# Optimization experiments

Measured on AMD Instinct MI355X. Metric: run time of the kernel, lower is better.

## Reference

```python
import jax, jax.numpy as jnp
import numpy as np

N = 50000       # nodes
E = 800000      # edges (avg degree 16)
IN = 256        # input features
HEADS = 4
D = 32          # per-head dim (hidden_channels/heads = 128/4)
HID = HEADS * D # 128
OUT = 64        # out_channels, last layer has 1 head
SLOPE = 0.2     # DGL GATConv LeakyReLU negative slope


def setup_inputs() -> dict:
    key = jax.random.key(0)
    ks = jax.random.split(key, 11)
    s = 0.05
    return {
        "x": jax.random.normal(ks[0], (N, IN), jnp.float32),
        "W1": jax.random.normal(ks[1], (IN, HID), jnp.float32) * s,
        "al1": jax.random.normal(ks[2], (HEADS, D), jnp.float32) * s,
        "ar1": jax.random.normal(ks[3], (HEADS, D), jnp.float32) * s,
        "b1": jnp.zeros((HID,), jnp.float32),
        "W2": jax.random.normal(ks[4], (HID, OUT), jnp.float32) * s,
        "al2": jax.random.normal(ks[5], (1, OUT), jnp.float32) * s,
        "ar2": jax.random.normal(ks[6], (1, OUT), jnp.float32) * s,
        "b2": jnp.zeros((OUT,), jnp.float32),
        "src": jax.random.randint(ks[7], (E,), 0, N),
        "dst": jax.random.randint(ks[8], (E,), 0, N),
    }


def gat_conv(h, W, al, ar, b, src, dst, heads, d):
    # h: [N, F_in]; projects, computes edge attention, edge-softmax over dst,
    # scatter-reduce aggregation. Matches dglnn.GATConv (bias, no residual).
    feat = (h @ W).reshape(-1, heads, d)              # [N, H, D]
    el = jnp.einsum('nhd,hd->nh', feat, al)           # [N, H]
    er = jnp.einsum('nhd,hd->nh', feat, ar)           # [N, H]
    e = jax.nn.leaky_relu(el[src] + er[dst], SLOPE)   # [E, H] edge scores
    # edge softmax over incoming edges of each dst node
    m = jax.ops.segment_max(e, dst, num_segments=N)   # [N, H]
    ee = jnp.exp(e - m[dst])                          # [E, H]
    z = jax.ops.segment_sum(ee, dst, num_segments=N)  # [N, H]
    a = ee / z[dst]                                   # [E, H]
    msg = feat[src] * a[:, :, None]                   # [E, H, D] gather + weight
    out = jax.ops.segment_sum(msg, dst, num_segments=N)  # [N, H, D]
    return out + b.reshape(heads, d)


def reference(x, W1, al1, ar1, b1, W2, al2, ar2, b2, src, dst):
    h = gat_conv(x, W1, al1, ar1, b1, src, dst, HEADS, D)   # [N, 4, 32]
    h = jax.nn.relu(h).reshape(N, HID)                      # activation; dropout=identity (eval)
    h = gat_conv(h, W2, al2, ar2, b2, src, dst, 1, OUT)     # [N, 1, 64]
    return h.reshape(N, OUT)
```

## Files before the change

kernel.cpp:

```cpp
#include <hip/hip_runtime.h>
#include <math.h>

#define NN   50000
#define EE   800000
#define INF_ 256
#define HID  128
#define OUTF 64
#define DCAP 96
#define SLOPE 0.2f
#define G1B  782
#define NB   391
#define NCH  196
#define CHCAP 6144

typedef __attribute__((ext_vector_type(8))) short short8v;
typedef __attribute__((ext_vector_type(4))) float f32x4;

__device__ __forceinline__ float lrelu(float x) { return x > 0.f ? x : SLOPE * x; }
__device__ __forceinline__ float4 lrelu4(float4 v) {
  v.x = lrelu(v.x); v.y = lrelu(v.y); v.z = lrelu(v.z); v.w = lrelu(v.w); return v;
}
__device__ __forceinline__ unsigned short f2bf(float x) {
  unsigned int u = __float_as_uint(x);
  unsigned int r = (u + 0x7FFFu + ((u >> 16) & 1u)) >> 16;
  return (unsigned short)r;
}

__global__ __launch_bounds__(256) void convW_k(const float* __restrict__ W1,
                                               const float* __restrict__ W2,
                                               unsigned short* __restrict__ W1T,
                                               unsigned short* __restrict__ W2T,
                                               int* __restrict__ cursor) {
  int t = threadIdx.x;
  if (blockIdx.x == 160) {
    if (t < NCH) cursor[t] = t * CHCAP;
    return;
  }
  int id = blockIdx.x * 256 + t;
  if (id < 32768) {
    int k = id >> 7, c = id & 127;
    W1T[c * 256 + k] = f2bf(W1[k * 128 + c]);
  } else {
    int i2 = id - 32768;
    if (i2 < 8192) {
      int k = i2 >> 6, c = i2 & 63;
      W2T[c * 128 + k] = f2bf(W2[i2]);
    }
  }
}

__global__ __launch_bounds__(256) void scat2_k(const int* __restrict__ src,
                                               const int* __restrict__ dst,
                                               int* __restrict__ cursor,
                                               int* __restrict__ packed) {
  __shared__ int h[NCH];
  __shared__ int cur[NCH];
  int t = threadIdx.x, b = blockIdx.x;
  if (t < NCH) h[t] = 0;
  __syncthreads();
  const int4* d4p = (const int4*)dst;
  const int4* s4p = (const int4*)src;
  int4 d4[2], s4[2];
  bool val[2];
#pragma unroll
  for (int it = 0; it < 2; ++it) {
    int qi = b * 512 + it * 256 + t;
    val[it] = qi < EE / 4;
    if (val[it]) {
      d4[it] = d4p[qi];
      s4[it] = s4p[qi];
      atomicAdd(&h[d4[it].x >> 8], 1);
      atomicAdd(&h[d4[it].y >> 8], 1);
      atomicAdd(&h[d4[it].z >> 8], 1);
      atomicAdd(&h[d4[it].w >> 8], 1);
    }
  }
  __syncthreads();
  if (t < NCH) {
    int c = h[t];
    cur[t] = (c > 0) ? atomicAdd(&cursor[t], c) : 0;
  }
  __syncthreads();
#pragma unroll
  for (int it = 0; it < 2; ++it) {
    if (val[it]) {
      int p, c, lim;
      c = d4[it].x >> 8; lim = (c + 1) * CHCAP;
      p = atomicAdd(&cur[c], 1); if (p < lim) packed[p] = (s4[it].x << 8) | (d4[it].x & 255);
      c = d4[it].y >> 8; lim = (c + 1) * CHCAP;
      p = atomicAdd(&cur[c], 1); if (p < lim) packed[p] = (s4[it].y << 8) | (d4[it].y & 255);
      c = d4[it].z >> 8; lim = (c + 1) * CHCAP;
      p = atomicAdd(&cur[c], 1); if (p < lim) packed[p] = (s4[it].z << 8) | (d4[it].z & 255);
      c = d4[it].w >> 8; lim = (c + 1) * CHCAP;
      p = atomicAdd(&cur[c], 1); if (p < lim) packed[p] = (s4[it].w << 8) | (d4[it].w & 255);
    }
  }
}

__global__ __launch_bounds__(256) void csort_k(const int* __restrict__ packed,
                                               const int* __restrict__ cursor,
                                               int* __restrict__ adj,
                                               int* __restrict__ rowptr,
                                               int* __restrict__ cnt) {
  __shared__ int pk[CHCAP];
  __shared__ int h[256], sc[256], cur[256];
  int t = threadIdx.x, b = blockIdx.x;
  int base = b * CHCAP;
  int len = cursor[b] - base; if (len > CHCAP) len = CHCAP;
  h[t] = 0;
  __syncthreads();
  for (int i = t; i < len; i += 256) {
    int v = packed[base + i];
    pk[i] = v;
    atomicAdd(&h[v & 255], 1);
  }
  __syncthreads();
  int v0 = h[t];
  sc[t] = v0;
  __syncthreads();
  for (int off = 1; off < 256; off <<= 1) {
    int add = (t >= off) ? sc[t - off] : 0;
    __syncthreads();
    sc[t] += add;
    __syncthreads();
  }
  int excl = sc[t] - v0;
  int node = b * 256 + t;
  if (node < NN) { cnt[node] = v0; rowptr[node] = base + excl; }
  cur[t] = excl;
  __syncthreads();
  for (int i = t; i < len; i += 256) {
    int v = pk[i];
    int p = atomicAdd(&cur[v & 255], 1);
    adj[base + p] = v & 0xFFFFFF00;
  }
}

__global__ __launch_bounds__(256) void g1s_k(const float* __restrict__ x,
                                             const unsigned short* __restrict__ W1T,
                                             unsigned short* __restrict__ featb,
                                             const float* __restrict__ al,
                                             const float* __restrict__ ar,
                                             float* __restrict__ el,
                                             float* __restrict__ er) {
  __shared__ unsigned short As[64 * 128];
  __shared__ unsigned short Bs[128 * 128];
  int t = threadIdx.x;
  int lane = t & 63, wid = t >> 6;
  int n0 = blockIdx.x * 64;
  int wr = (wid >> 1) * 32;
  int wc = (wid & 1) * 64;

  f32x4 acc[2][4];
#pragma unroll
  for (int m = 0; m < 2; ++m)
#pragma unroll
    for (int n = 0; n < 4; ++n) acc[m][n] = (f32x4){0.f, 0.f, 0.f, 0.f};

  for (int pass = 0; pass < 2; ++pass) {
    int k0 = pass * 128;
#pragma unroll
    for (int it = 0; it < 8; ++it) {
      int f = it * 256 + t;
      int row = f >> 5;
      int c4  = f & 31;
      int grow = n0 + row;
      float4 v = make_float4(0.f, 0.f, 0.f, 0.f);
      if (grow < NN) v = *(const float4*)&x[grow * INF_ + k0 + c4 * 4];
      ushort4 b4;
      b4.x = f2bf(v.x); b4.y = f2bf(v.y); b4.z = f2bf(v.z); b4.w = f2bf(v.w);
      int byte = row * 256 + c4 * 8;
      byte ^= (row & 15) << 4;
      *(ushort4*)((char*)As + byte) = b4;
    }
#pragma unroll
    for (int it = 0; it < 8; ++it) {
      int f = it * 256 + t;
      int c  = f >> 4;
      int k8 = f & 15;
      uint4 v = *(const uint4*)&W1T[c * 256 + k0 + k8 * 8];
      int byte = c * 256 + k8 * 16;
      byte ^= (c & 15) << 4;
      *(uint4*)((char*)Bs + byte) = v;
    }
    __syncthreads();
#pragma unroll
    for (int ks = 0; ks < 4; ++ks) {
      int kb = ks * 64 + (lane >> 4) * 16;
      short8v a[2], b[4];
#pragma unroll
      for (int m = 0; m < 2; ++m) {
        int row = wr + m * 16 + (lane & 15);
        int byte = (row * 256 + kb) ^ ((row & 15) << 4);
        a[m] = *(const short8v*)((const char*)As + byte);
      }
#pragma unroll
      for (int n = 0; n < 4; ++n) {
        int c = wc + n * 16 + (lane & 15);
        int byte = (c * 256 + kb) ^ ((c & 15) << 4);
        b[n] = *(const short8v*)((const char*)Bs + byte);
      }
#pragma unroll
      for (int m = 0; m < 2; ++m)
#pragma unroll
        for (int n = 0; n < 4; ++n)
          acc[m][n] = __builtin_amdgcn_mfma_f32_16x16x32_bf16(a[m], b[n], acc[m][n], 0, 0, 0);
    }
    __syncthreads();
  }
#pragma unroll
  for (int m = 0; m < 2; ++m) {
    int rbase = wr + m * 16 + (lane >> 4) * 4;
#pragma unroll
    for (int r = 0; r < 4; ++r)
#pragma unroll
      for (int n = 0; n < 4; ++n)
        As[(rbase + r) * 128 + wc + n * 16 + (lane & 15)] = f2bf(acc[m][n][r]);
  }
  __syncthreads();
#pragma unroll
  for (int it = 0; it < 4; ++it) {
    int id = it * 256 + t;
    int row = id >> 4, c8 = id & 15;
    int grow = n0 + row;
    if (grow < NN)
      *(uint4*)&featb[grow * HID + c8 * 8] = *(const uint4*)&As[row * 128 + c8 * 8];
  }
  {
    int row = t >> 2, h = t & 3;
    int grow = n0 + row;
    float pe = 0.f, pr = 0.f;
#pragma unroll
    for (int d = 0; d < 16; ++d) {
      unsigned int u = *(const unsigned int*)&As[row * 128 + h * 32 + d * 2];
      float f0 = __uint_as_float(u << 16);
      float f1 = __uint_as_float(u & 0xFFFF0000u);
      float2 a2 = *(const float2*)&al[h * 32 + d * 2];
      float2 r2 = *(const float2*)&ar[h * 32 + d * 2];
      pe += f0 * a2.x + f1 * a2.y;
      pr += f0 * r2.x + f1 * r2.y;
    }
    if (grow < NN) { el[grow * 4 + h] = pe; er[grow * 4 + h] = pr; }
  }
}

__global__ __launch_bounds__(256) void agg1_k(const unsigned short* __restrict__ featb,
                                              const float* __restrict__ el1,
                                              const float* __restrict__ er1,
                                              const float* __restrict__ b1,
                                              const int* __restrict__ cnt,
                                              const int* __restrict__ rowptr,
                                              const int* __restrict__ adj,
                                              unsigned short* __restrict__ houtb) {
  __shared__ float ee[4][DCAP * 4];
  int wid = threadIdx.x >> 6, lane = threadIdx.x & 63;
  int n = blockIdx.x * 4 + wid;
  int deg = cnt[n]; if (deg > DCAP) deg = DCAP;
  const int* bk = adj + rowptr[n];
  float4 er = *(const float4*)(er1 + n * 4);
  int hl = lane >> 4;
  int m64 = deg < 64 ? deg : 64;
  int myoff = (lane < m64) ? bk[lane] : -1;
  const char* fb = (const char*)featb;
  int lb = lane * 4;

  float4 e4my = make_float4(0.f, 0.f, 0.f, 0.f);
  if (myoff >= 0 && deg <= 64)
    e4my = *(const float4*)((const char*)el1 + (myoff >> 4));
  unsigned int upre[16];
#pragma unroll
  for (int k = 0; k < 16; ++k) {
    int o = __shfl(myoff, k);
    upre[k] = *(const unsigned int*)(fb + ((k < m64) ? o : 0) + lb);
  }
  __builtin_amdgcn_sched_barrier(0);

  if (deg <= 64) {
    float4 ex = make_float4(0.f, 0.f, 0.f, 0.f);
    if (myoff >= 0) {
      float4 sc = lrelu4(make_float4(e4my.x + er.x, e4my.y + er.y,
                                     e4my.z + er.z, e4my.w + er.w));
      ex = make_float4(__expf(sc.x), __expf(sc.y), __expf(sc.z), __expf(sc.w));
    }
    float4 zs = ex;
#pragma unroll
    for (int off = 1; off < 64; off <<= 1) {
      zs.x += __shfl_xor(zs.x, off); zs.y += __shfl_xor(zs.y, off);
      zs.z += __shfl_xor(zs.z, off); zs.w += __shfl_xor(zs.w, off);
    }
    if (myoff >= 0) {
      float4 w = make_float4(ex.x / zs.x, ex.y / zs.y, ex.z / zs.z, ex.w / zs.w);
      *(float4*)&ee[wid][lane * 4] = w;
    }
  } else {
    float4 mx = make_float4(-INFINITY, -INFINITY, -INFINITY, -INFINITY);
    for (int j = lane; j < deg; j += 64) {
      int o = bk[j];
      float4 e4 = *(const float4*)((const char*)el1 + (o >> 4));
      float4 sc = lrelu4(make_float4(e4.x + er.x, e4.y + er.y, e4.z + er.z, e4.w + er.w));
      mx.x = fmaxf(mx.x, sc.x); mx.y = fmaxf(mx.y, sc.y);
      mx.z = fmaxf(mx.z, sc.z); mx.w = fmaxf(mx.w, sc.w);
    }
#pragma unroll
    for (int off = 1; off < 64; off <<= 1) {
      mx.x = fmaxf(mx.x, __shfl_xor(mx.x, off));
      mx.y = fmaxf(mx.y, __shfl_xor(mx.y, off));
      mx.z = fmaxf(mx.z, __shfl_xor(mx.z, off));
      mx.w = fmaxf(mx.w, __shfl_xor(mx.w, off));
    }
    float4 zs = make_float4(0.f, 0.f, 0.f, 0.f);
    for (int j = lane; j < deg; j += 64) {
      int o = bk[j];
      float4 e4 = *(const float4*)((const char*)el1 + (o >> 4));
      float4 sc = lrelu4(make_float4(e4.x + er.x, e4.y + er.y, e4.z + er.z, e4.w + er.w));
      float4 ex = make_float4(__expf(sc.x - mx.x), __expf(sc.y - mx.y),
                              __expf(sc.z - mx.z), __expf(sc.w - mx.w));
      *(float4*)&ee[wid][j * 4] = ex;
      zs.x += ex.x; zs.y += ex.y; zs.z += ex.z; zs.w += ex.w;
    }
#pragma unroll
    for (int off = 1; off < 64; off <<= 1) {
      zs.x += __shfl_xor(zs.x, off); zs.y += __shfl_xor(zs.y, off);
      zs.z += __shfl_xor(zs.z, off); zs.w += __shfl_xor(zs.w, off);
    }
    float4 iz = make_float4(1.f / zs.x, 1.f / zs.y, 1.f / zs.z, 1.f / zs.w);
    for (int j = lane; j < deg; j += 64) {
      float4 t = *(const float4*)&ee[wid][j * 4];
      t.x *= iz.x; t.y *= iz.y; t.z *= iz.z; t.w *= iz.w;
      *(float4*)&ee[wid][j * 4] = t;
    }
  }

  float acc0 = 0.f, acc1 = 0.f;
#pragma unroll
  for (int k = 0; k < 16; ++k) {
    float w = (k < m64) ? ee[wid][k * 4 + hl] : 0.f;
    acc0 += __uint_as_float(upre[k] << 16) * w;
    acc1 += __uint_as_float(upre[k] & 0xFFFF0000u) * w;
  }
  int j = 16;
  for (; j + 16 <= m64; j += 16) {
    unsigned int u[16];
#pragma unroll
    for (int q = 0; q < 16; ++q) {
      int o = __shfl(myoff, j + q);
      u[q] = *(const unsigned int*)(fb + o + lb);
    }
#pragma unroll
    for (int q = 0; q < 16; ++q) {
      float w = ee[wid][(j + q) * 4 + hl];
      acc0 += __uint_as_float(u[q] << 16) * w;
      acc1 += __uint_as_float(u[q] & 0xFFFF0000u) * w;
    }
  }
  for (; j + 4 <= m64; j += 4) {
    unsigned int u[4];
#pragma unroll
    for (int q = 0; q < 4; ++q) {
      int o = __shfl(myoff, j + q);
      u[q] = *(const unsigned int*)(fb + o + lb);
    }
#pragma unroll
    for (int q = 0; q < 4; ++q) {
      float w = ee[wid][(j + q) * 4 + hl];
      acc0 += __uint_as_float(u[q] << 16) * w;
      acc1 += __uint_as_float(u[q] & 0xFFFF0000u) * w;
    }
  }
  for (; j < m64; ++j) {
    int o = __shfl(myoff, j);
    unsigned int u = *(const unsigned int*)(fb + o + lb);
    float w = ee[wid][j * 4 + hl];
    acc0 += __uint_as_float(u << 16) * w; acc1 += __uint_as_float(u & 0xFFFF0000u) * w;
  }
  for (; j < deg; ++j) {
    int o = bk[j];
    unsigned int u = *(const unsigned int*)(fb + o + lb);
    float w = ee[wid][j * 4 + hl];
    acc0 += __uint_as_float(u << 16) * w; acc1 += __uint_as_float(u & 0xFFFF0000u) * w;
  }
  float2 bb = *(const float2*)&b1[lane * 2];
  float o0 = fmaxf(acc0 + bb.x, 0.f);
  float o1 = fmaxf(acc1 + bb.y, 0.f);
  unsigned int p = (unsigned int)f2bf(o0) | ((unsigned int)f2bf(o1) << 16);
  *(unsigned int*)&houtb[n * HID + lane * 2] = p;
}

__global__ __launch_bounds__(256) void gemm2s_mfma(const unsigned short* __restrict__ hb,
                                                   const unsigned short* __restrict__ W2T,
                                                   unsigned short* __restrict__ f2b,
                                                   const float* __restrict__ al2,
                                                   const float* __restrict__ ar2,
                                                   float* __restrict__ el2,
                                                   float* __restrict__ er2) {
  __shared__ char smem[32768];
  __shared__ float pel[64][4], per_[64][4];
  unsigned short* As = (unsigned short*)smem;
  unsigned short* Bs = (unsigned short*)(smem + 16384);
  int t = threadIdx.x, lane = t & 63, wid = t >> 6;
  int n0 = blockIdx.x * 64;
  f32x4 acc[4];
#pragma unroll
  for (int n = 0; n < 4; ++n) acc[n] = (f32x4){0.f, 0.f, 0.f, 0.f};

#pragma unroll
  for (int it = 0; it < 4; ++it) {
    int id = it * 256 + t;
    int row = id >> 4, c8 = id & 15;
    int grow = n0 + row;
    uint4 v = make_uint4(0, 0, 0, 0);
    if (grow < NN) v = *(const uint4*)&hb[grow * HID + c8 * 8];
    int byte = row * 256 + c8 * 16;
    byte ^= (row & 15) << 4;
    *(uint4*)((char*)As + byte) = v;
  }
#pragma unroll
  for (int it = 0; it < 4; ++it) {
    int id = it * 256 + t;
    int row = id >> 4, c8 = id & 15;
    uint4 v = *(const uint4*)&W2T[row * 128 + c8 * 8];
    int byte = row * 256 + c8 * 16;
    byte ^= (row & 15) << 4;
    *(uint4*)((char*)Bs + byte) = v;
  }
  __syncthreads();
  int wr = wid * 16;
#pragma unroll
  for (int ks = 0; ks < 4; ++ks) {
    int kb = ks * 64 + (lane >> 4) * 16;
    int arow = wr + (lane & 15);
    int abyte = (arow * 256 + kb) ^ ((arow & 15) << 4);
    short8v a = *(const short8v*)((const char*)As + abyte);
#pragma unroll
    for (int n = 0; n < 4; ++n) {
      int c = n * 16 + (lane & 15);
      int bbyte = (c * 256 + kb) ^ ((c & 15) << 4);
      short8v b = *(const short8v*)((const char*)Bs + bbyte);
      acc[n] = __builtin_amdgcn_mfma_f32_16x16x32_bf16(a, b, acc[n], 0, 0, 0);
    }
  }
  __syncthreads();
  float* stg = (float*)smem;
  unsigned short* sB = (unsigned short*)(smem + 16640);
  int rloc = wr + (lane >> 4) * 4;
#pragma unroll
  for (int r = 0; r < 4; ++r) {
#pragma unroll
    for (int n = 0; n < 4; ++n) {
      int col = n * 16 + (lane & 15);
      float v = acc[n][r];
      stg[(rloc + r) * 65 + col] = v;
      sB[(rloc + r) * 64 + col] = f2bf(v);
    }
  }
  __syncthreads();
#pragma unroll
  for (int it = 0; it < 2; ++it) {
    int id = it * 256 + t;
    int row = id >> 3, c8 = id & 7;
    int grow = n0 + row;
    if (grow < NN)
      *(uint4*)&f2b[grow * OUTF + c8 * 8] = *(const uint4*)&sB[row * 64 + c8 * 8];
  }
  {
    int row = t >> 2, seg = t & 3;
    float pe = 0.f, pr = 0.f;
#pragma unroll
    for (int d = 0; d < 16; ++d) {
      int c = seg * 16 + d;
      float f = stg[row * 65 + c];
      pe += f * al2[c];
      pr += f * ar2[c];
    }
    pel[row][seg] = pe; per_[row][seg] = pr;
  }
  __syncthreads();
  if (t < 64) {
    int grow = n0 + t;
    if (grow < NN) {
      el2[grow] = pel[t][0] + pel[t][1] + pel[t][2] + pel[t][3];
      er2[grow] = per_[t][0] + per_[t][1] + per_[t][2] + per_[t][3];
    }
  }
}

__global__ __launch_bounds__(256) void agg2_k(const unsigned short* __restrict__ f2b,
                                              const float* __restrict__ el2,
                                              const float* __restrict__ er2,
                                              const float* __restrict__ b2,
                                              const int* __restrict__ cnt,
                                              const int* __restrict__ rowptr,
                                              const int* __restrict__ adj,
                                              float* __restrict__ out) {
  __shared__ float ee[4][DCAP];
  int wid = threadIdx.x >> 6, lane = threadIdx.x & 63;
  int n = blockIdx.x * 4 + wid;
  int deg = cnt[n]; if (deg > DCAP) deg = DCAP;
  const int* bk = adj + rowptr[n];
  float er = er2[n];
  int m64 = deg < 64 ? deg : 64;
  int myoff = (lane < m64) ? bk[lane] : -1;
  int half = lane >> 5, c2 = (lane & 31) * 2;
  const char* fb = (const char*)f2b;

  float elmy = 0.f;
  if (myoff >= 0 && deg <= 64)
    elmy = *(const float*)((const char*)el2 + (myoff >> 6));
  unsigned int upre[8];
#pragma unroll
  for (int s = 0; s < 8; ++s) {
    int je = s * 2 + half;
    int o = __shfl(myoff, je);
    upre[s] = *(const unsigned int*)(fb + ((je < m64) ? (o >> 1) : 0) + c2 * 2);
  }
  __builtin_amdgcn_sched_barrier(0);

  if (deg <= 64) {
    float ex = (myoff >= 0) ? __expf(lrelu(elmy + er)) : 0.f;
    float zs = ex;
#pragma unroll
    for (int off = 1; off < 64; off <<= 1) zs += __shfl_xor(zs, off);
    if (myoff >= 0) ee[wid][lane] = ex / zs;
  } else {
    float mx = -INFINITY;
    for (int j = lane; j < deg; j += 64) {
      int o = bk[j];
      mx = fmaxf(mx, lrelu(*(const float*)((const char*)el2 + (o >> 6)) + er));
    }
#pragma unroll
    for (int off = 1; off < 64; off <<= 1) mx = fmaxf(mx, __shfl_xor(mx, off));
    float zs = 0.f;
    for (int j = lane; j < deg; j += 64) {
      int o = bk[j];
      float ex = __expf(lrelu(*(const float*)((const char*)el2 + (o >> 6)) + er) - mx);
      ee[wid][j] = ex;
      zs += ex;
    }
#pragma unroll
    for (int off = 1; off < 64; off <<= 1) zs += __shfl_xor(zs, off);
    float iz = 1.f / zs;
    for (int j = lane; j < deg; j += 64) ee[wid][j] *= iz;
  }

  float acc0 = 0.f, acc1 = 0.f;
#pragma unroll
  for (int s = 0; s < 8; ++s) {
    int je = s * 2 + half;
    float w = (je < m64) ? ee[wid][je] : 0.f;
    acc0 += __uint_as_float(upre[s] << 16) * w;
    acc1 += __uint_as_float(upre[s] & 0xFFFF0000u) * w;
  }
  int j = 16;
  for (; j + 16 <= deg; j += 16) {
    unsigned int u[8]; float w[8];
#pragma unroll
    for (int q = 0; q < 8; ++q) {
      int je = j + q * 2 + half;
      int os = __shfl(myoff, je < 64 ? je : 63);
      int o = (je < 64) ? os : bk[je];
      u[q] = *(const unsigned int*)(fb + (o >> 1) + c2 * 2);
      w[q] = ee[wid][je];
    }
#pragma unroll
    for (int q = 0; q < 8; ++q) {
      acc0 += __uint_as_float(u[q] << 16) * w[q];
      acc1 += __uint_as_float(u[q] & 0xFFFF0000u) * w[q];
    }
  }
  for (; j < deg; j += 2) {
    int je = j + half;
    int os = __shfl(myoff, (je < 64) ? je : 63);
    float w = 0.f; unsigned int u = 0;
    if (je < deg) {
      int o = (je < 64) ? os : bk[je];
      u = *(const unsigned int*)(fb + (o >> 1) + c2 * 2);
      w = ee[wid][je];
    }
    acc0 += __uint_as_float(u << 16) * w;
    acc1 += __uint_as_float(u & 0xFFFF0000u) * w;
  }
  acc0 += __shfl_xor(acc0, 32);
  acc1 += __shfl_xor(acc1, 32);
  if (lane < 32) {
    float2 bb = *(const float2*)&b2[c2];
    *(float2*)&out[n * OUTF + c2] = make_float2(acc0 + bb.x, acc1 + bb.y);
  }
}

extern "C" void kernel_launch(void* const* d_in, const int* in_sizes, int n_in,
                              void* d_out, int out_size, void* d_ws, size_t ws_size,
                              hipStream_t stream) {
  const float* x   = (const float*)d_in[0];
  const float* W1  = (const float*)d_in[1];
  const float* al1 = (const float*)d_in[2];
  const float* ar1 = (const float*)d_in[3];
  const float* b1  = (const float*)d_in[4];
  const float* W2  = (const float*)d_in[5];
  const float* al2 = (const float*)d_in[6];
  const float* ar2 = (const float*)d_in[7];
  const float* b2  = (const float*)d_in[8];
  const int*   src = (const int*)d_in[9];
  const int*   dst = (const int*)d_in[10];
  float* out = (float*)d_out;

  char* base = (char*)d_ws;
  unsigned short* feat1b = (unsigned short*)base;
  unsigned short* f2b    = (unsigned short*)base;
  int*            packed = (int*)base;
  unsigned short* hb     = (unsigned short*)(base + 12800000);
  float* el1 = (float*)(base + 25600000);
  float* er1 = el1 + NN * 4;
  float* el2 = er1 + NN * 4;
  float* er2 = el2 + NN;
  int* cnt    = (int*)(er2 + NN);
  int* rowptr = cnt + NN;
  int* adj    = rowptr + NN;
  int* cursor = adj + NCH * CHCAP;
  unsigned short* W1T = (unsigned short*)(cursor + NCH);
  unsigned short* W2T = W1T + 256 * 128;

  convW_k <<<161, 256, 0, stream>>>(W1, W2, W1T, W2T, cursor);
  scat2_k <<<NB, 256, 0, stream>>>(src, dst, cursor, packed);
  csort_k <<<NCH, 256, 0, stream>>>(packed, cursor, adj, rowptr, cnt);
  g1s_k   <<<G1B, 256, 0, stream>>>(x, W1T, feat1b, al1, ar1, el1, er1);
  agg1_k  <<<NN / 4, 256, 0, stream>>>(feat1b, el1, er1, b1, cnt, rowptr, adj, hb);
  gemm2s_mfma<<<G1B, 256, 0, stream>>>(hb, W2T, f2b, al2, ar2, el2, er2);
  agg2_k  <<<NN / 4, 256, 0, stream>>>(f2b, el2, er2, b2, cnt, rowptr, adj, out);
}
```

Baseline: 125.9 us.

## Merge graph-prep and GEMM kernels to cut launches and overlap independent work

Fuses the weight conversion into the edge-scatter kernel and the per-chunk counting sort into the first-layer GEMM kernel, selecting the role by block index. The cursor initialization moves to a memset, with cursors now relative to each chunk base. The packed buffer gets its own workspace region instead of aliasing feat1b, because the sort and the GEMM now run concurrently. This removes two launches and lets independent blocks overlap. The cost is one shared 48KB smem allocation per block, which may reduce occupancy for the sort blocks.

```diff
diff --git a/kernel.cpp b/kernel.cpp
--- a/kernel.cpp
+++ b/kernel.cpp
@@ -26,36 +26,32 @@
   return (unsigned short)r;
 }
 
-__global__ __launch_bounds__(256) void convW_k(const float* __restrict__ W1,
-                                               const float* __restrict__ W2,
-                                               unsigned short* __restrict__ W1T,
-                                               unsigned short* __restrict__ W2T,
-                                               int* __restrict__ cursor) {
+__global__ __launch_bounds__(256) void prep_k(const int* __restrict__ src,
+                                              const int* __restrict__ dst,
+                                              int* __restrict__ cursor,
+                                              int* __restrict__ packed,
+                                              const float* __restrict__ W1,
+                                              const float* __restrict__ W2,
+                                              unsigned short* __restrict__ W1T,
+                                              unsigned short* __restrict__ W2T) {
   int t = threadIdx.x;
-  if (blockIdx.x == 160) {
-    if (t < NCH) cursor[t] = t * CHCAP;
+  if (blockIdx.x >= NB) {
+    int id = (blockIdx.x - NB) * 256 + t;
+    if (id < 32768) {
+      int k = id >> 7, c = id & 127;
+      W1T[c * 256 + k] = f2bf(W1[k * 128 + c]);
+    } else {
+      int i2 = id - 32768;
+      if (i2 < 8192) {
+        int k = i2 >> 6, c = i2 & 63;
+        W2T[c * 128 + k] = f2bf(W2[i2]);
+      }
+    }
     return;
   }
-  int id = blockIdx.x * 256 + t;
-  if (id < 32768) {
-    int k = id >> 7, c = id & 127;
-    W1T[c * 256 + k] = f2bf(W1[k * 128 + c]);
-  } else {
-    int i2 = id - 32768;
-    if (i2 < 8192) {
-      int k = i2 >> 6, c = i2 & 63;
-      W2T[c * 128 + k] = f2bf(W2[i2]);
-    }
-  }
-}
-
-__global__ __launch_bounds__(256) void scat2_k(const int* __restrict__ src,
-                                               const int* __restrict__ dst,
-                                               int* __restrict__ cursor,
-                                               int* __restrict__ packed) {
   __shared__ int h[NCH];
   __shared__ int cur[NCH];
-  int t = threadIdx.x, b = blockIdx.x;
+  int b = blockIdx.x;
   if (t < NCH) h[t] = 0;
   __syncthreads();
   const int4* d4p = (const int4*)dst;
@@ -78,7 +74,7 @@
   __syncthreads();
   if (t < NCH) {
     int c = h[t];
-    cur[t] = (c > 0) ? atomicAdd(&cursor[t], c) : 0;
+    cur[t] = t * CHCAP + ((c > 0) ? atomicAdd(&cursor[t], c) : 0);
   }
   __syncthreads();
 #pragma unroll
@@ -97,57 +93,63 @@
   }
 }
 
-__global__ __launch_bounds__(256) void csort_k(const int* __restrict__ packed,
-                                               const int* __restrict__ cursor,
-                                               int* __restrict__ adj,
-                                               int* __restrict__ rowptr,
-                                               int* __restrict__ cnt) {
-  __shared__ int pk[CHCAP];
-  __shared__ int h[256], sc[256], cur[256];
-  int t = threadIdx.x, b = blockIdx.x;
-  int base = b * CHCAP;
-  int len = cursor[b] - base; if (len > CHCAP) len = CHCAP;
-  h[t] = 0;
-  __syncthreads();
-  for (int i = t; i < len; i += 256) {
-    int v = packed[base + i];
-    pk[i] = v;
-    atomicAdd(&h[v & 255], 1);
-  }
-  __syncthreads();
-  int v0 = h[t];
-  sc[t] = v0;
-  __syncthreads();
-  for (int off = 1; off < 256; off <<= 1) {
-    int add = (t >= off) ? sc[t - off] : 0;
-    __syncthreads();
-    sc[t] += add;
-    __syncthreads();
-  }
-  int excl = sc[t] - v0;
-  int node = b * 256 + t;
-  if (node < NN) { cnt[node] = v0; rowptr[node] = base + excl; }
-  cur[t] = excl;
-  __syncthreads();
-  for (int i = t; i < len; i += 256) {
-    int v = pk[i];
-    int p = atomicAdd(&cur[v & 255], 1);
-    adj[base + p] = v & 0xFFFFFF00;
-  }
-}
-
-__global__ __launch_bounds__(256) void g1s_k(const float* __restrict__ x,
+__global__ __launch_bounds__(256) void cg1_k(const int* __restrict__ packed,
+                                             const int* __restrict__ cursor,
+                                             int* __restrict__ adj,
+                                             int* __restrict__ rowptr,
+                                             int* __restrict__ cnt,
+                                             const float* __restrict__ x,
                                              const unsigned short* __restrict__ W1T,
                                              unsigned short* __restrict__ featb,
                                              const float* __restrict__ al,
                                              const float* __restrict__ ar,
                                              float* __restrict__ el,
                                              float* __restrict__ er) {
-  __shared__ unsigned short As[64 * 128];
-  __shared__ unsigned short Bs[128 * 128];
+  __shared__ char smem[49152];
   int t = threadIdx.x;
+
+  if (blockIdx.x < NCH) {
+    int* pk  = (int*)smem;
+    int* h   = (int*)(smem + 24576);
+    int* sc  = (int*)(smem + 25600);
+    int* cur = (int*)(smem + 26624);
+    int b = blockIdx.x;
+    int base = b * CHCAP;
+    int len = cursor[b]; if (len > CHCAP) len = CHCAP;
+    h[t] = 0;
+    __syncthreads();
+    for (int i = t; i < len; i += 256) {
+      int v = packed[base + i];
+      pk[i] = v;
+      atomicAdd(&h[v & 255], 1);
+    }
+    __syncthreads();
+    int v0 = h[t];
+    sc[t] = v0;
+    __syncthreads();
+    for (int off = 1; off < 256; off <<= 1) {
+      int add = (t >= off) ? sc[t - off] : 0;
+      __syncthreads();
+      sc[t] += add;
+      __syncthreads();
+    }
+    int excl = sc[t] - v0;
+    int node = b * 256 + t;
+    if (node < NN) { cnt[node] = v0; rowptr[node] = base + excl; }
+    cur[t] = excl;
+    __syncthreads();
+    for (int i = t; i < len; i += 256) {
+      int v = pk[i];
+      int p = atomicAdd(&cur[v & 255], 1);
+      adj[base + p] = v & 0xFFFFFF00;
+    }
+    return;
+  }
+
+  unsigned short* As = (unsigned short*)smem;
+  unsigned short* Bs = (unsigned short*)(smem + 16384);
   int lane = t & 63, wid = t >> 6;
-  int n0 = blockIdx.x * 64;
+  int n0 = (blockIdx.x - NCH) * 64;
   int wr = (wid >> 1) * 32;
   int wc = (wid & 1) * 64;
 
@@ -227,20 +229,20 @@
       *(uint4*)&featb[grow * HID + c8 * 8] = *(const uint4*)&As[row * 128 + c8 * 8];
   }
   {
-    int row = t >> 2, h = t & 3;
+    int row = t >> 2, hh = t & 3;
     int grow = n0 + row;
     float pe = 0.f, pr = 0.f;
 #pragma unroll
     for (int d = 0; d < 16; ++d) {
-      unsigned int u = *(const unsigned int*)&As[row * 128 + h * 32 + d * 2];
+      unsigned int u = *(const unsigned int*)&As[row * 128 + hh * 32 + d * 2];
       float f0 = __uint_as_float(u << 16);
       float f1 = __uint_as_float(u & 0xFFFF0000u);
-      float2 a2 = *(const float2*)&al[h * 32 + d * 2];
-      float2 r2 = *(const float2*)&ar[h * 32 + d * 2];
+      float2 a2 = *(const float2*)&al[hh * 32 + d * 2];
+      float2 r2 = *(const float2*)&ar[hh * 32 + d * 2];
       pe += f0 * a2.x + f1 * a2.y;
       pr += f0 * r2.x + f1 * r2.y;
     }
-    if (grow < NN) { el[grow * 4 + h] = pe; er[grow * 4 + h] = pr; }
+    if (grow < NN) { el[grow * 4 + hh] = pe; er[grow * 4 + hh] = pr; }
   }
 }
 
@@ -606,7 +608,6 @@
   char* base = (char*)d_ws;
   unsigned short* feat1b = (unsigned short*)base;
   unsigned short* f2b    = (unsigned short*)base;
-  int*            packed = (int*)base;
   unsigned short* hb     = (unsigned short*)(base + 12800000);
   float* el1 = (float*)(base + 25600000);
   float* er1 = el1 + NN * 4;
@@ -615,15 +616,16 @@
   int* cnt    = (int*)(er2 + NN);
   int* rowptr = cnt + NN;
   int* adj    = rowptr + NN;
-  int* cursor = adj + NCH * CHCAP;
+  int* packed = adj + NCH * CHCAP;
+  int* cursor = packed + NCH * CHCAP;
   unsigned short* W1T = (unsigned short*)(cursor + NCH);
   unsigned short* W2T = W1T + 256 * 128;
 
-  convW_k <<<161, 256, 0, stream>>>(W1, W2, W1T, W2T, cursor);
-  scat2_k <<<NB, 256, 0, stream>>>(src, dst, cursor, packed);
-  csort_k <<<NCH, 256, 0, stream>>>(packed, cursor, adj, rowptr, cnt);
-  g1s_k   <<<G1B, 256, 0, stream>>>(x, W1T, feat1b, al1, ar1, el1, er1);
-  agg1_k  <<<NN / 4, 256, 0, stream>>>(feat1b, el1, er1, b1, cnt, rowptr, adj, hb);
+  hipMemsetAsync(cursor, 0, NCH * sizeof(int), stream);
+  prep_k <<<NB + 161, 256, 0, stream>>>(src, dst, cursor, packed, W1, W2, W1T, W2T);
+  cg1_k  <<<NCH + G1B, 256, 0, stream>>>(packed, cursor, adj, rowptr, cnt,
+                                         x, W1T, feat1b, al1, ar1, el1, er1);
+  agg1_k <<<NN / 4, 256, 0, stream>>>(feat1b, el1, er1, b1, cnt, rowptr, adj, hb);
   gemm2s_mfma<<<G1B, 256, 0, stream>>>(hb, W2T, f2b, al2, ar2, el2, er2);
-  agg2_k  <<<NN / 4, 256, 0, stream>>>(f2b, el2, er2, b2, cnt, rowptr, adj, out);
-}
+  agg2_k <<<NN / 4, 256, 0, stream>>>(f2b, el2, er2, b2, cnt, rowptr, adj, out);
+}
```

Result: faster. 115.4 us, median of 2 (-8.3%).
